# Performance work log

Measured on AMD Instinct MI355X. Metric: run time of the kernel, lower is better.

Reference implementation:

```python
import jax, jax.numpy as jnp
import numpy as np
import itertools

B, RES, RES_, STRIDE = 256, 14, 7, 2
N, N_ = RES * RES, RES_ * RES_
IN_DIM, OUT_DIM = 384, 512
H, KD, AR = 12, 32, 2
D = AR * KD            # 64, per-head value dim
DH = D * H             # 768
NH_KD = KD * H         # 384
KV_H = DH + NH_KD      # 1152
EPS = 1e-5


def _bias_idxs():
    # Replicates the relative-offset indexing from __init__.
    points = list(itertools.product(range(RES), range(RES)))
    points_ = list(itertools.product(range(RES_), range(RES_)))
    offsets, idxs = {}, []
    for p1 in points_:
        for p2 in points:
            off = (abs(p1[0] * STRIDE - p2[0]), abs(p1[1] * STRIDE - p2[1]))
            if off not in offsets:
                offsets[off] = len(offsets)
            idxs.append(offsets[off])
    return np.array(idxs, dtype=np.int32).reshape(N_, N), len(offsets)


def linear_bn(x, w, gamma, beta, mean, var):
    # Linear (no bias) followed by BatchNorm1d in inference form (fused affine).
    s = gamma / jnp.sqrt(var + EPS)
    return jnp.matmul(x, w.T) * s + (beta - mean * s)


def setup_inputs() -> dict:
    key = jax.random.key(0)
    ks = jax.random.split(key, 12)
    idxs_np, n_off = _bias_idxs()

    def bn_params(k, dim):
        k1, k2, k3, k4 = jax.random.split(k, 4)
        return (jax.random.normal(k1, (dim,)) * 0.1 + 1.0,   # gamma
                jax.random.normal(k2, (dim,)) * 0.1,          # beta
                jax.random.normal(k3, (dim,)) * 0.1,          # running_mean
                jax.random.uniform(k4, (dim,), minval=0.5, maxval=1.5))  # running_var

    kv_g, kv_b, kv_m, kv_v = bn_params(ks[1], KV_H)
    q_g, q_b, q_m, q_v = bn_params(ks[3], NH_KD)
    pr_g, pr_b, pr_m, pr_v = bn_params(ks[5], OUT_DIM)

    return {
        "x": jax.random.normal(ks[0], (B, N, IN_DIM), dtype=jnp.float32),
        "kv_w": jax.random.normal(ks[6], (KV_H, IN_DIM), dtype=jnp.float32) * (IN_DIM ** -0.5),
        "kv_g": kv_g, "kv_b": kv_b, "kv_m": kv_m, "kv_v": kv_v,
        "q_w": jax.random.normal(ks[7], (NH_KD, IN_DIM), dtype=jnp.float32) * (IN_DIM ** -0.5),
        "q_g": q_g, "q_b": q_b, "q_m": q_m, "q_v": q_v,
        "proj_w": jax.random.normal(ks[8], (OUT_DIM, DH), dtype=jnp.float32) * (DH ** -0.5),
        "proj_g": pr_g, "proj_b": pr_b, "proj_m": pr_m, "proj_v": pr_v,
        "attention_biases": jax.random.normal(ks[9], (H, n_off), dtype=jnp.float32) * 0.02,
        "bias_idxs": jnp.asarray(idxs_np),
    }


def reference(x, kv_w, kv_g, kv_b, kv_m, kv_v,
              q_w, q_g, q_b, q_m, q_v,
              proj_w, proj_g, proj_b, proj_m, proj_v,
              attention_biases, bias_idxs):
    Bsz = x.shape[0]
    scale = KD ** -0.5
    # kv projection: [B, N, H, KD+D] -> split into k, v
    kv = linear_bn(x, kv_w, kv_g, kv_b, kv_m, kv_v).reshape(Bsz, N, H, KD + D)
    k, v = kv[..., :KD], kv[..., KD:]
    # strided subsample of queries: [B, 14, 14, C] -> [B, 49, C]
    xs = x.reshape(Bsz, RES, RES, IN_DIM)[:, ::STRIDE, ::STRIDE].reshape(Bsz, N_, IN_DIM)
    q = linear_bn(xs, q_w, q_g, q_b, q_m, q_v).reshape(Bsz, N_, H, KD)
    # attention with gathered relative-position bias: bias [H, N_, N]
    bias = attention_biases[:, bias_idxs]
    attn = jnp.einsum('bqhd,bkhd->bhqk', q, k) * scale + bias
    attn = jax.nn.softmax(attn, axis=-1)
    out = jnp.einsum('bhqk,bkhd->bqhd', attn, v).reshape(Bsz, N_, DH)
    out = jax.nn.hard_swish(out)
    return linear_bn(out, proj_w, proj_g, proj_b, proj_m, proj_v)
```

## Files before the change

kernel.cpp:

```cpp
#include <hip/hip_runtime.h>
#include <hip/hip_bf16.h>
#include <math.h>

typedef unsigned short U16;
typedef unsigned int U32;
typedef __attribute__((ext_vector_type(8))) short bf8;
typedef __attribute__((ext_vector_type(4))) float f4;
typedef __attribute__((ext_vector_type(4))) unsigned short u16x4;

#define AS1 __attribute__((address_space(1)))
#define AS3 __attribute__((address_space(3)))

#define BSZ   256
#define NTOK  196
#define NQ    49
#define INDIM 384
#define OUTD  512
#define NH    12
#define DV    64
#define DHD   768
#define KVH   1152
#define NPADR 224

__device__ inline U16 f2bf(float f){
    __hip_bfloat16 h = __float2bfloat16(f);
    return *(U16*)&h;
}
__device__ inline f4 f4zero(){ f4 z; z[0]=0.f; z[1]=0.f; z[2]=0.f; z[3]=0.f; return z; }
__device__ inline bf8 bf8zero(){ bf8 v;
#pragma unroll
    for (int j=0;j<8;++j) v[j]=0; return v; }

__global__ void k_cast8p(const float* __restrict__ in, U16* __restrict__ out, int n8){
    int i = blockIdx.x*256 + threadIdx.x;
    if (i >= n8) return;
    int rall = i / 48;
    int c8   = i - rall*48;
    int b    = rall / NPADR;
    int r    = rall - b*NPADR;
    U16 o[8];
    if (r < NTOK){
        const float* p = in + ((size_t)(b*NTOK + r))*INDIM + c8*8;
#pragma unroll
        for (int j=0;j<8;++j) o[j] = f2bf(p[j]);
    } else {
#pragma unroll
        for (int j=0;j<8;++j) o[j] = 0;
    }
    *(bf8*)(out + (size_t)i*8) = *(const bf8*)o;
}

__global__ void k_castxs(const float* __restrict__ x, U16* __restrict__ out, int n8){
    int i = blockIdx.x*256 + threadIdx.x;
    if (i >= n8) return;
    int row = i / 48;
    int c8  = i - row*48;
    int b   = row / 49;
    int q   = row - b*49;
    int r_  = q / 7, c_ = q - r_*7;
    const float* p = x + ((size_t)(b*NTOK + 28*r_ + 2*c_))*INDIM + c8*8;
    U16 o[8];
#pragma unroll
    for (int j=0;j<8;++j) o[j] = f2bf(p[j]);
    *(bf8*)(out + (size_t)i*8) = *(const bf8*)o;
}

#define W1C (KVH*INDIM/8)
#define W2C (INDIM*INDIM/8)
#define W3C (OUTD*DHD/8)
__global__ void k_castw(const float* __restrict__ w1, const float* __restrict__ w2,
                        const float* __restrict__ w3, U16* __restrict__ o1,
                        U16* __restrict__ o2, U16* __restrict__ o3){
    int i = blockIdx.x*256 + threadIdx.x;
    const float* p; U16* o;
    if (i < W1C){ p = w1 + (size_t)i*8; o = o1 + (size_t)i*8; }
    else if (i < W1C+W2C){ int k=i-W1C; p = w2 + (size_t)k*8; o = o2 + (size_t)k*8; }
    else if (i < W1C+W2C+W3C){ int k=i-W1C-W2C; p = w3 + (size_t)k*8; o = o3 + (size_t)k*8; }
    else return;
    U16 t[8];
#pragma unroll
    for (int j=0;j<8;++j) t[j] = f2bf(p[j]);
    *(bf8*)o = *(const bf8*)t;
}

#define BIAS_N   (NH*NQ*NTOK)
#define BIAS_BLK ((BIAS_N+255)/256)
#define BN_BLK   ((KVH+INDIM+OUTD)/256)
__global__ void k_misc(const float* __restrict__ ab, const int* __restrict__ idxs, int n_off,
                       const float* __restrict__ g1, const float* __restrict__ b1,
                       const float* __restrict__ m1, const float* __restrict__ v1,
                       const float* __restrict__ g2, const float* __restrict__ b2,
                       const float* __restrict__ m2, const float* __restrict__ v2,
                       const float* __restrict__ g3, const float* __restrict__ b3,
                       const float* __restrict__ m3, const float* __restrict__ v3,
                       float* __restrict__ s1, float* __restrict__ bo1,
                       float* __restrict__ s2, float* __restrict__ bo2,
                       float* __restrict__ s3, float* __restrict__ bo3,
                       float* __restrict__ bias_out){
    int blk = blockIdx.x;
    int tid = threadIdx.x;
    if (blk < BIAS_BLK){
        int i = blk*256 + tid;
        if (i < BIAS_N){
            int h = i / (NQ*NTOK);
            int qk = i - h*(NQ*NTOK);
            bias_out[i] = ab[h*n_off + idxs[qk]];
        }
    } else {
        int i = (blk-BIAS_BLK)*256 + tid;
        const float *g,*b,*m,*v; float *so,*bo; int k;
        if (i < KVH){ g=g1;b=b1;m=m1;v=v1;so=s1;bo=bo1;k=i; }
        else if (i < KVH+INDIM){ g=g2;b=b2;m=m2;v=v2;so=s2;bo=bo2;k=i-KVH; }
        else { g=g3;b=b3;m=m3;v=v3;so=s3;bo=bo3;k=i-KVH-INDIM; }
        float s = g[k] / sqrtf(v[k] + 1e-5f);
        so[k] = s;
        bo[k] = b[k] - m[k]*s;
    }
}

#define KLO 12800
__global__ __launch_bounds__(256,2) void k_fused(
    const U16* __restrict__ xbf, const U16* __restrict__ kvw, const U16* __restrict__ qo_,
    const float* __restrict__ skv, const float* __restrict__ bkv,
    const float* __restrict__ biasf, U16* __restrict__ aout)
{
    __shared__ U16 smem[20480];
    const int hw = blockIdx.x;
    const int bh = (hw & 7)*384 + (hw >> 3);
    const int b = bh / NH, h = bh - b*NH;
    const int tid = threadIdx.x, lane = tid & 63, w = tid >> 6;
    const int wm = w & 1, wn = w >> 1;
    const int l15 = lane & 15, oct = lane >> 4;

    U16* Ab[2] = { smem + 0,     smem + 7168 };
    U16* Bb[2] = { smem + 14336, smem + 17408 };

    U32 aoff[4];
#pragma unroll
    for (int c=0;c<3;++c){
        int s = c*256 + tid;
        int ach = s / NPADR, ar = s - ach*NPADR;
        aoff[c] = (U32)(b*NPADR + ar)*INDIM + ach*8;
    }
    {
        int s = 768 + (tid & 127);
        int ach = s / NPADR, ar = s - ach*NPADR;
        aoff[3] = (U32)(b*NPADR + ar)*INDIM + ach*8;
    }
    U32 boff[2];
    {
        int s0 = tid;
        int bc0 = s0 / 96, br0 = s0 - bc0*96;
        boff[0] = (U32)(h*96 + br0)*INDIM + bc0*8;
        int s1 = 128 + (tid | 128);
        int bc1 = s1 / 96, br1 = s1 - bc1*96;
        boff[1] = (U32)(h*96 + br1)*INDIM + bc1*8;
    }

    f4 acc[7][3];
#pragma unroll
    for (int i=0;i<7;++i)
#pragma unroll
        for (int j=0;j<3;++j) acc[i][j] = f4zero();

#define STAGE(buf, kb) do{ \
    _Pragma("unroll") \
    for (int c=0;c<3;++c) \
        __builtin_amdgcn_global_load_lds((const AS1 U32*)(xbf + aoff[c] + (kb)), \
            (AS3 U32*)(Ab[buf] + (c*256+tid)*8), 16, 0, 0); \
    if (tid < 128) \
        __builtin_amdgcn_global_load_lds((const AS1 U32*)(xbf + aoff[3] + (kb)), \
            (AS3 U32*)(Ab[buf] + (768+tid)*8), 16, 0, 0); \
    __builtin_amdgcn_global_load_lds((const AS1 U32*)(kvw + boff[0] + (kb)), \
        (AS3 U32*)(Bb[buf] + tid*8), 16, 0, 0); \
    if (tid >= 128) \
        __builtin_amdgcn_global_load_lds((const AS1 U32*)(kvw + boff[1] + (kb)), \
            (AS3 U32*)(Bb[buf] + (128+tid)*8), 16, 0, 0); \
}while(0)

    STAGE(0, 0);

#pragma unroll
    for (int kt=0; kt<12; ++kt){
        const int cur = kt & 1;
        if (kt < 11){
            STAGE(cur^1, (kt+1)*32);
            asm volatile("s_waitcnt vmcnt(5)" ::: "memory");
        } else {
            asm volatile("s_waitcnt vmcnt(0)" ::: "memory");
        }
        __builtin_amdgcn_sched_barrier(0);
        __builtin_amdgcn_s_barrier();
        __builtin_amdgcn_sched_barrier(0);

        bf8 af[7], bfr[3];
#pragma unroll
        for (int i=0;i<7;++i)
            af[i]  = *(const bf8*)(Ab[cur] + (oct*NPADR + wm*112 + i*16 + l15)*8);
#pragma unroll
        for (int j=0;j<3;++j)
            bfr[j] = *(const bf8*)(Bb[cur] + (oct*96 + wn*48 + j*16 + l15)*8);
        __builtin_amdgcn_s_setprio(1);
#pragma unroll
        for (int i=0;i<7;++i)
#pragma unroll
            for (int j=0;j<3;++j)
                acc[i][j] = __builtin_amdgcn_mfma_f32_16x16x32_bf16(af[i], bfr[j], acc[i][j], 0, 0, 0);
        __builtin_amdgcn_s_setprio(0);
        __builtin_amdgcn_sched_barrier(0);
        __builtin_amdgcn_s_barrier();
        __builtin_amdgcn_sched_barrier(0);
    }
#undef STAGE

#pragma unroll
    for (int j=0;j<3;++j){
        const int cc = wn*48 + j*16 + l15;
        const float sc = skv[h*96 + cc];
        const float bi = bkv[h*96 + cc];
#pragma unroll
        for (int i=0;i<7;++i){
            const int n0 = wm*112 + i*16 + oct*4;
            if (cc < 32){
#pragma unroll
                for (int r=0;r<4;++r)
                    smem[KLO + ((cc>>3)*NPADR + n0 + r)*8 + (cc&7)] = f2bf(acc[i][j][r]*sc + bi);
            } else if (n0 < 200){
                const int dv = cc - 32;
                u16x4 pk;
#pragma unroll
                for (int r=0;r<4;++r) pk[r] = f2bf(acc[i][j][r]*sc + bi);
                *(u16x4*)(smem + ((n0>>3)*64 + dv)*8 + (oct&1)*4) = pk;
            }
        }
    }
    __syncthreads();

    const int qg = w*16 + l15;
    bf8 qf = bf8zero();
    if (qg < NQ) qf = *(const bf8*)(qo_ + ((size_t)(b*NQ + qg))*INDIM + h*32 + oct*8);

    f4 sacc[14];
#pragma unroll
    for (int mt=0;mt<14;++mt) sacc[mt] = f4zero();
#pragma unroll
    for (int mt=0;mt<14;++mt){
        const bf8 kf = *(const bf8*)(smem + KLO + (oct*NPADR + mt*16 + l15)*8);
        sacc[mt] = __builtin_amdgcn_mfma_f32_16x16x32_bf16(kf, qf, sacc[mt], 0, 0, 0);
    }

    const float scale = 0.17677669529663689f;
    float mx = -1e30f;
#pragma unroll
    for (int mt=0;mt<14;++mt){
        const int n0 = mt*16 + oct*4;
        f4 bi4 = f4zero();
        if (qg < NQ && n0 < NTOK) bi4 = *(const f4*)(biasf + ((size_t)h*NQ + qg)*NTOK + n0);
#pragma unroll
        for (int r=0;r<4;++r){
            float s = (n0 + r < NTOK) ? sacc[mt][r]*scale + bi4[r] : -1e30f;
            sacc[mt][r] = s;
            mx = fmaxf(mx, s);
        }
    }
    mx = fmaxf(mx, __shfl_xor(mx, 16));
    mx = fmaxf(mx, __shfl_xor(mx, 32));

    float sum = 0.f;
#pragma unroll
    for (int mt=0;mt<14;++mt){
#pragma unroll
        for (int r=0;r<4;++r){
            float p = (mt*16 + oct*4 + r < NTOK) ? __expf(sacc[mt][r] - mx) : 0.f;
            sacc[mt][r] = p;
            sum += p;
        }
    }
    sum += __shfl_xor(sum, 16);
    sum += __shfl_xor(sum, 32);
    const float inv = 1.f / sum;

    const int src1 = l15 + (oct & 1)*32;
    const int src2 = src1 + 16;
    const bool hiT = (oct >> 1) != 0;
    f4 pacc[4];
#pragma unroll
    for (int dt=0;dt<4;++dt) pacc[dt] = f4zero();
#pragma unroll
    for (int kt=0;kt<7;++kt){
        const int m0 = 2*kt, m1 = 2*kt+1;
        U32 q00 = (U32)f2bf(sacc[m0][0]*inv) | ((U32)f2bf(sacc[m0][1]*inv) << 16);
        U32 q01 = (U32)f2bf(sacc[m0][2]*inv) | ((U32)f2bf(sacc[m0][3]*inv) << 16);
        U32 q10 = (U32)f2bf(sacc[m1][0]*inv) | ((U32)f2bf(sacc[m1][1]*inv) << 16);
        U32 q11 = (U32)f2bf(sacc[m1][2]*inv) | ((U32)f2bf(sacc[m1][3]*inv) << 16);
        U32 a0 = __shfl(q00, src1), a1 = __shfl(q01, src1);
        U32 c0 = __shfl(q10, src1), c1 = __shfl(q11, src1);
        U32 b0 = __shfl(q00, src2), b1 = __shfl(q01, src2);
        U32 d0 = __shfl(q10, src2), d1 = __shfl(q11, src2);
        union { U32 u[4]; bf8 v; } pu;
        pu.u[0] = hiT ? c0 : a0;
        pu.u[1] = hiT ? c1 : a1;
        pu.u[2] = hiT ? d0 : b0;
        pu.u[3] = hiT ? d1 : b1;
#pragma unroll
        for (int dt=0;dt<4;++dt){
            const bf8 vf = *(const bf8*)(smem + ((kt*4 + oct)*64 + dt*16 + l15)*8);
            pacc[dt] = __builtin_amdgcn_mfma_f32_16x16x32_bf16(pu.v, vf, pacc[dt], 0, 0, 0);
        }
    }

#pragma unroll
    for (int dt=0;dt<4;++dt){
#pragma unroll
        for (int r=0;r<4;++r){
            const int qo2 = w*16 + oct*4 + r;
            if (qo2 < NQ){
                const int d = dt*16 + l15;
                float v = pacc[dt][r];
                float tt = fminf(fmaxf(v + 3.f, 0.f), 6.f);
                aout[((size_t)(b*NQ + qo2))*DHD + h*DV + d] = f2bf(v * tt * (1.f/6.f));
            }
        }
    }
}

__global__ __launch_bounds__(256,2) void k_qgemm(
    const U16* __restrict__ A, const U16* __restrict__ Bw,
    const float* __restrict__ s_arr, const float* __restrict__ b_arr,
    U16* __restrict__ o16)
{
    __shared__ U16 smem[32768];
    U16* Ab[2] = { smem,          smem + 8192 };
    U16* Bb[2] = { smem + 16384,  smem + 24576 };
    const int gn0 = blockIdx.x * 128;
    const int gm0 = blockIdx.y * 128;
    const int tid  = threadIdx.x;
    const int lane = tid & 63;
    const int w    = tid >> 6;
    const int wm   = w >> 1, wn = w & 1;
    const int l15  = lane & 15, oct = lane >> 4;

    f4 acc[4][4];
#pragma unroll
    for (int i=0;i<4;++i)
#pragma unroll
        for (int j=0;j<4;++j) acc[i][j] = f4zero();

    size_t aoff[4], boff[4];
#pragma unroll
    for (int c=0;c<4;++c){
        int slot = c*256 + tid;
        int row = slot & 127, ch = slot >> 7;
        aoff[c] = (size_t)(gm0 + row)*INDIM + ch*8;
        boff[c] = (size_t)(gn0 + row)*INDIM + ch*8;
    }

#pragma unroll
    for (int c=0;c<4;++c){
        __builtin_amdgcn_global_load_lds((const AS1 U32*)(A + aoff[c]),
            (AS3 U32*)(Ab[0] + (c*256+tid)*8), 16, 0, 0);
        __builtin_amdgcn_global_load_lds((const AS1 U32*)(Bw + boff[c]),
            (AS3 U32*)(Bb[0] + (c*256+tid)*8), 16, 0, 0);
    }

#pragma unroll
    for (int kt=0; kt<6; ++kt){
        const int cur = kt & 1;
        if (kt+1 < 6){
            const int kb = (kt+1)*64;
#pragma unroll
            for (int c=0;c<4;++c){
                __builtin_amdgcn_global_load_lds((const AS1 U32*)(A + aoff[c] + kb),
                    (AS3 U32*)(Ab[cur^1] + (c*256+tid)*8), 16, 0, 0);
                __builtin_amdgcn_global_load_lds((const AS1 U32*)(Bw + boff[c] + kb),
                    (AS3 U32*)(Bb[cur^1] + (c*256+tid)*8), 16, 0, 0);
            }
            asm volatile("s_waitcnt vmcnt(8)" ::: "memory");
        } else {
            asm volatile("s_waitcnt vmcnt(0)" ::: "memory");
        }
        __builtin_amdgcn_sched_barrier(0);
        __builtin_amdgcn_s_barrier();
        __builtin_amdgcn_sched_barrier(0);

#pragma unroll
        for (int kk=0;kk<2;++kk){
            bf8 af[4], bfr[4];
#pragma unroll
            for (int i=0;i<4;++i)
                af[i]  = *(const bf8*)(Ab[cur] + ((kk*4+oct)*128 + wm*64 + i*16 + l15)*8);
#pragma unroll
            for (int j=0;j<4;++j)
                bfr[j] = *(const bf8*)(Bb[cur] + ((kk*4+oct)*128 + wn*64 + j*16 + l15)*8);
            __builtin_amdgcn_s_setprio(1);
#pragma unroll
            for (int i=0;i<4;++i)
#pragma unroll
                for (int j=0;j<4;++j)
                    acc[i][j] = __builtin_amdgcn_mfma_f32_16x16x32_bf16(af[i], bfr[j], acc[i][j], 0, 0, 0);
            __builtin_amdgcn_s_setprio(0);
        }
        __builtin_amdgcn_sched_barrier(0);
        __builtin_amdgcn_s_barrier();
        __builtin_amdgcn_sched_barrier(0);
    }

#pragma unroll
    for (int j=0;j<4;++j){
        const int col = gn0 + wn*64 + j*16 + l15;
        const float sc = s_arr[col];
        const float bi = b_arr[col];
#pragma unroll
        for (int i=0;i<4;++i){
            const int row0 = gm0 + wm*64 + i*16 + oct*4;
#pragma unroll
            for (int r=0;r<4;++r)
                o16[(size_t)(row0+r)*INDIM + col] = f2bf(acc[i][j][r]*sc + bi);
        }
    }
}

__global__ __launch_bounds__(256,2) void k_proj(
    const U16* __restrict__ A, const U16* __restrict__ Bw,
    const float* __restrict__ s_arr, const float* __restrict__ b_arr,
    float* __restrict__ o32)
{
    __shared__ U16 smem[32768];
    U16* Ab[2] = { smem,          smem + 8192 };
    U16* Bb[2] = { smem + 16384,  smem + 24576 };
    const int l   = (blockIdx.x & 7)*49 + (blockIdx.x >> 3);
    const int gn0 = (l & 3) * 128;
    const int gm0 = (l >> 2) * 128;
    const int tid  = threadIdx.x;
    const int lane = tid & 63;
    const int w    = tid >> 6;
    const int wm   = w >> 1, wn = w & 1;
    const int l15  = lane & 15, oct = lane >> 4;

    f4 acc[4][4];
#pragma unroll
    for (int i=0;i<4;++i)
#pragma unroll
        for (int j=0;j<4;++j) acc[i][j] = f4zero();

    size_t aoff[4], boff[4];
#pragma unroll
    for (int c=0;c<4;++c){
        int slot = c*256 + tid;
        int row = slot & 127, ch = slot >> 7;
        aoff[c] = (size_t)(gm0 + row)*DHD + ch*8;
        boff[c] = (size_t)(gn0 + row)*DHD + ch*8;
    }

#pragma unroll
    for (int c=0;c<4;++c){
        __builtin_amdgcn_global_load_lds((const AS1 U32*)(A + aoff[c]),
            (AS3 U32*)(Ab[0] + (c*256+tid)*8), 16, 0, 0);
        __builtin_amdgcn_global_load_lds((const AS1 U32*)(Bw + boff[c]),
            (AS3 U32*)(Bb[0] + (c*256+tid)*8), 16, 0, 0);
    }

#pragma unroll
    for (int kt=0; kt<12; ++kt){
        const int cur = kt & 1;
        if (kt+1 < 12){
            const int kb = (kt+1)*64;
#pragma unroll
            for (int c=0;c<4;++c){
                __builtin_amdgcn_global_load_lds((const AS1 U32*)(A + aoff[c] + kb),
                    (AS3 U32*)(Ab[cur^1] + (c*256+tid)*8), 16, 0, 0);
                __builtin_amdgcn_global_load_lds((const AS1 U32*)(Bw + boff[c] + kb),
                    (AS3 U32*)(Bb[cur^1] + (c*256+tid)*8), 16, 0, 0);
            }
            asm volatile("s_waitcnt vmcnt(8)" ::: "memory");
        } else {
            asm volatile("s_waitcnt vmcnt(0)" ::: "memory");
        }
        __builtin_amdgcn_sched_barrier(0);
        __builtin_amdgcn_s_barrier();
        __builtin_amdgcn_sched_barrier(0);

#pragma unroll
        for (int kk=0;kk<2;++kk){
            bf8 af[4], bfr[4];
#pragma unroll
            for (int i=0;i<4;++i)
                af[i]  = *(const bf8*)(Ab[cur] + ((kk*4+oct)*128 + wm*64 + i*16 + l15)*8);
#pragma unroll
            for (int j=0;j<4;++j)
                bfr[j] = *(const bf8*)(Bb[cur] + ((kk*4+oct)*128 + wn*64 + j*16 + l15)*8);
            __builtin_amdgcn_s_setprio(1);
#pragma unroll
            for (int i=0;i<4;++i)
#pragma unroll
                for (int j=0;j<4;++j)
                    acc[i][j] = __builtin_amdgcn_mfma_f32_16x16x32_bf16(af[i], bfr[j], acc[i][j], 0, 0, 0);
            __builtin_amdgcn_s_setprio(0);
        }
        __builtin_amdgcn_sched_barrier(0);
        __builtin_amdgcn_s_barrier();
        __builtin_amdgcn_sched_barrier(0);
    }

#pragma unroll
    for (int j=0;j<4;++j){
        const int col = gn0 + wn*64 + j*16 + l15;
        const float sc = s_arr[col];
        const float bi = b_arr[col];
#pragma unroll
        for (int i=0;i<4;++i){
            const int row0 = gm0 + wm*64 + i*16 + oct*4;
#pragma unroll
            for (int r=0;r<4;++r)
                o32[(size_t)(row0+r)*OUTD + col] = acc[i][j][r]*sc + bi;
        }
    }
}

extern "C" void kernel_launch(void* const* d_in, const int* in_sizes, int n_in,
                              void* d_out, int out_size, void* d_ws, size_t ws_size,
                              hipStream_t stream)
{
    const float* x    = (const float*)d_in[0];
    const float* kv_w = (const float*)d_in[1];
    const float* kv_g = (const float*)d_in[2];
    const float* kv_b = (const float*)d_in[3];
    const float* kv_m = (const float*)d_in[4];
    const float* kv_v = (const float*)d_in[5];
    const float* q_w  = (const float*)d_in[6];
    const float* q_g  = (const float*)d_in[7];
    const float* q_b  = (const float*)d_in[8];
    const float* q_m  = (const float*)d_in[9];
    const float* q_v  = (const float*)d_in[10];
    const float* pr_w = (const float*)d_in[11];
    const float* pr_g = (const float*)d_in[12];
    const float* pr_b = (const float*)d_in[13];
    const float* pr_m = (const float*)d_in[14];
    const float* pr_v = (const float*)d_in[15];
    const float* ab   = (const float*)d_in[16];
    const int*  idxs  = (const int*)d_in[17];
    const int n_off = in_sizes[16] / NH;

    char* ws = (char*)d_ws;
    size_t off = 0;
    auto alloc = [&](size_t bytes)->char*{
        char* p = ws + off; off += (bytes + 255) & ~(size_t)255; return p;
    };
    U16*   x_bf   = (U16*)  alloc((size_t)BSZ*NPADR*INDIM*2);
    U16*   xs_bf  = (U16*)  alloc((size_t)BSZ*NQ*INDIM*2);
    U16*   kvw_bf = (U16*)  alloc((size_t)KVH*INDIM*2);
    U16*   qw_bf  = (U16*)  alloc((size_t)INDIM*INDIM*2);
    U16*   prw_bf = (U16*)  alloc((size_t)OUTD*DHD*2);
    float* s_kv   = (float*)alloc(KVH*4);
    float* b_kv   = (float*)alloc(KVH*4);
    float* s_q    = (float*)alloc(INDIM*4);
    float* b_q    = (float*)alloc(INDIM*4);
    float* s_pr   = (float*)alloc(OUTD*4);
    float* b_pr   = (float*)alloc(OUTD*4);
    float* biasf  = (float*)alloc(((size_t)NH*NQ*NTOK + 256)*4);
    U16*   q_out  = (U16*)  alloc((size_t)BSZ*NQ*INDIM*2);
    U16*   a_out  = (U16*)  alloc((size_t)BSZ*NQ*DHD*2);
    if (off > ws_size) return;

    {
        int n8 = BSZ*NPADR*INDIM/8;
        k_cast8p<<<(n8+255)/256, 256, 0, stream>>>(x, x_bf, n8);
    }
    {
        int n8 = BSZ*NQ*INDIM/8;
        k_castxs<<<(n8+255)/256, 256, 0, stream>>>(x, xs_bf, n8);
    }
    k_castw<<<(W1C+W2C+W3C+255)/256, 256, 0, stream>>>(kv_w, q_w, pr_w, kvw_bf, qw_bf, prw_bf);
    k_misc<<<BIAS_BLK+BN_BLK, 256, 0, stream>>>(
        ab, idxs, n_off,
        kv_g, kv_b, kv_m, kv_v, q_g, q_b, q_m, q_v, pr_g, pr_b, pr_m, pr_v,
        s_kv, b_kv, s_q, b_q, s_pr, b_pr, biasf);

    {
        dim3 g(INDIM/128, BSZ*NQ/128);
        k_qgemm<<<g, 256, 0, stream>>>(xs_bf, qw_bf, s_q, b_q, q_out);
    }
    k_fused<<<BSZ*NH, 256, 0, stream>>>(x_bf, kvw_bf, q_out, s_kv, b_kv, biasf, a_out);
    k_proj<<<392, 256, 0, stream>>>(a_out, prw_bf, s_pr, b_pr, (float*)d_out);
}
```

Before: 191.3 us.

## Unify q and proj GEMMs into 128x64-tile template, fold query subsampling into loads

```diff
diff --git a/kernel.cpp b/kernel.cpp
--- a/kernel.cpp
+++ b/kernel.cpp
@@ -47,21 +47,6 @@
 #pragma unroll
         for (int j=0;j<8;++j) o[j] = 0;
     }
-    *(bf8*)(out + (size_t)i*8) = *(const bf8*)o;
-}
-
-__global__ void k_castxs(const float* __restrict__ x, U16* __restrict__ out, int n8){
-    int i = blockIdx.x*256 + threadIdx.x;
-    if (i >= n8) return;
-    int row = i / 48;
-    int c8  = i - row*48;
-    int b   = row / 49;
-    int q   = row - b*49;
-    int r_  = q / 7, c_ = q - r_*7;
-    const float* p = x + ((size_t)(b*NTOK + 28*r_ + 2*c_))*INDIM + c8*8;
-    U16 o[8];
-#pragma unroll
-    for (int j=0;j<8;++j) o[j] = f2bf(p[j]);
     *(bf8*)(out + (size_t)i*8) = *(const bf8*)o;
 }
 
@@ -324,58 +309,70 @@
     }
 }
 
-__global__ __launch_bounds__(256,2) void k_qgemm(
+template<int EPI, int NK, int KD, int NTILN, int NWG, bool SUB>
+__global__ __launch_bounds__(256,2) void k_g64(
     const U16* __restrict__ A, const U16* __restrict__ Bw,
     const float* __restrict__ s_arr, const float* __restrict__ b_arr,
-    U16* __restrict__ o16)
+    U16* __restrict__ o16, float* __restrict__ o32)
 {
-    __shared__ U16 smem[32768];
+    __shared__ U16 smem[24576];
     U16* Ab[2] = { smem,          smem + 8192 };
-    U16* Bb[2] = { smem + 16384,  smem + 24576 };
-    const int gn0 = blockIdx.x * 128;
-    const int gm0 = blockIdx.y * 128;
+    U16* Bb[2] = { smem + 16384,  smem + 20480 };
+    constexpr int QQ = NWG/8, RR = NWG%8;
+    const int xcd = blockIdx.x & 7, rest = blockIdx.x >> 3;
+    const int l = (xcd < RR ? xcd*(QQ+1) : RR*(QQ+1) + (xcd-RR)*QQ) + rest;
+    const int mtl = l / NTILN, ntl = l - mtl*NTILN;
+    const int gm0 = mtl*128, gn0 = ntl*64;
     const int tid  = threadIdx.x;
     const int lane = tid & 63;
     const int w    = tid >> 6;
-    const int wm   = w >> 1, wn = w & 1;
+    const int wm   = w & 1, wn = w >> 1;
     const int l15  = lane & 15, oct = lane >> 4;
 
-    f4 acc[4][4];
+    f4 acc[4][2];
 #pragma unroll
     for (int i=0;i<4;++i)
 #pragma unroll
-        for (int j=0;j<4;++j) acc[i][j] = f4zero();
-
-    size_t aoff[4], boff[4];
+        for (int j=0;j<2;++j) acc[i][j] = f4zero();
+
+    U32 aoff[4], boff[2];
 #pragma unroll
     for (int c=0;c<4;++c){
         int slot = c*256 + tid;
         int row = slot & 127, ch = slot >> 7;
-        aoff[c] = (size_t)(gm0 + row)*INDIM + ch*8;
-        boff[c] = (size_t)(gn0 + row)*INDIM + ch*8;
-    }
-
-#pragma unroll
-    for (int c=0;c<4;++c){
-        __builtin_amdgcn_global_load_lds((const AS1 U32*)(A + aoff[c]),
-            (AS3 U32*)(Ab[0] + (c*256+tid)*8), 16, 0, 0);
-        __builtin_amdgcn_global_load_lds((const AS1 U32*)(Bw + boff[c]),
-            (AS3 U32*)(Bb[0] + (c*256+tid)*8), 16, 0, 0);
-    }
-
-#pragma unroll
-    for (int kt=0; kt<6; ++kt){
+        int grow = gm0 + row;
+        if (SUB){
+            int b2 = grow / NQ, qq = grow - b2*NQ;
+            grow = b2*NPADR + 28*(qq/7) + 2*(qq%7);
+        }
+        aoff[c] = (U32)grow*KD + ch*8;
+    }
+#pragma unroll
+    for (int c=0;c<2;++c){
+        int slot = c*256 + tid;
+        int row = slot & 63, ch = slot >> 6;
+        boff[c] = (U32)(gn0 + row)*KD + ch*8;
+    }
+
+#define STG(buf, kb) do{ \
+    _Pragma("unroll") \
+    for (int c=0;c<4;++c) \
+        __builtin_amdgcn_global_load_lds((const AS1 U32*)(A + aoff[c] + (kb)), \
+            (AS3 U32*)(Ab[buf] + (c*256+tid)*8), 16, 0, 0); \
+    _Pragma("unroll") \
+    for (int c=0;c<2;++c) \
+        __builtin_amdgcn_global_load_lds((const AS1 U32*)(Bw + boff[c] + (kb)), \
+            (AS3 U32*)(Bb[buf] + (c*256+tid)*8), 16, 0, 0); \
+}while(0)
+
+    STG(0, 0);
+
+#pragma unroll
+    for (int kt=0; kt<NK; ++kt){
         const int cur = kt & 1;
-        if (kt+1 < 6){
-            const int kb = (kt+1)*64;
-#pragma unroll
-            for (int c=0;c<4;++c){
-                __builtin_amdgcn_global_load_lds((const AS1 U32*)(A + aoff[c] + kb),
-                    (AS3 U32*)(Ab[cur^1] + (c*256+tid)*8), 16, 0, 0);
-                __builtin_amdgcn_global_load_lds((const AS1 U32*)(Bw + boff[c] + kb),
-                    (AS3 U32*)(Bb[cur^1] + (c*256+tid)*8), 16, 0, 0);
-            }
-            asm volatile("s_waitcnt vmcnt(8)" ::: "memory");
+        if (kt+1 < NK){
+            STG(cur^1, (kt+1)*64);
+            asm volatile("s_waitcnt vmcnt(6)" ::: "memory");
         } else {
             asm volatile("s_waitcnt vmcnt(0)" ::: "memory");
         }
@@ -385,18 +382,18 @@
 
 #pragma unroll
         for (int kk=0;kk<2;++kk){
-            bf8 af[4], bfr[4];
+            bf8 af[4], bfr[2];
 #pragma unroll
             for (int i=0;i<4;++i)
                 af[i]  = *(const bf8*)(Ab[cur] + ((kk*4+oct)*128 + wm*64 + i*16 + l15)*8);
 #pragma unroll
-            for (int j=0;j<4;++j)
-                bfr[j] = *(const bf8*)(Bb[cur] + ((kk*4+oct)*128 + wn*64 + j*16 + l15)*8);
+            for (int j=0;j<2;++j)
+                bfr[j] = *(const bf8*)(Bb[cur] + ((kk*4+oct)*64 + wn*32 + j*16 + l15)*8);
             __builtin_amdgcn_s_setprio(1);
 #pragma unroll
             for (int i=0;i<4;++i)
 #pragma unroll
-                for (int j=0;j<4;++j)
+                for (int j=0;j<2;++j)
                     acc[i][j] = __builtin_amdgcn_mfma_f32_16x16x32_bf16(af[i], bfr[j], acc[i][j], 0, 0, 0);
             __builtin_amdgcn_s_setprio(0);
         }
@@ -404,115 +401,22 @@
         __builtin_amdgcn_s_barrier();
         __builtin_amdgcn_sched_barrier(0);
     }
-
-#pragma unroll
-    for (int j=0;j<4;++j){
-        const int col = gn0 + wn*64 + j*16 + l15;
+#undef STG
+
+#pragma unroll
+    for (int j=0;j<2;++j){
+        const int col = gn0 + wn*32 + j*16 + l15;
         const float sc = s_arr[col];
         const float bi = b_arr[col];
 #pragma unroll
         for (int i=0;i<4;++i){
             const int row0 = gm0 + wm*64 + i*16 + oct*4;
 #pragma unroll
-            for (int r=0;r<4;++r)
-                o16[(size_t)(row0+r)*INDIM + col] = f2bf(acc[i][j][r]*sc + bi);
-        }
-    }
-}
-
-__global__ __launch_bounds__(256,2) void k_proj(
-    const U16* __restrict__ A, const U16* __restrict__ Bw,
-    const float* __restrict__ s_arr, const float* __restrict__ b_arr,
-    float* __restrict__ o32)
-{
-    __shared__ U16 smem[32768];
-    U16* Ab[2] = { smem,          smem + 8192 };
-    U16* Bb[2] = { smem + 16384,  smem + 24576 };
-    const int l   = (blockIdx.x & 7)*49 + (blockIdx.x >> 3);
-    const int gn0 = (l & 3) * 128;
-    const int gm0 = (l >> 2) * 128;
-    const int tid  = threadIdx.x;
-    const int lane = tid & 63;
-    const int w    = tid >> 6;
-    const int wm   = w >> 1, wn = w & 1;
-    const int l15  = lane & 15, oct = lane >> 4;
-
-    f4 acc[4][4];
-#pragma unroll
-    for (int i=0;i<4;++i)
-#pragma unroll
-        for (int j=0;j<4;++j) acc[i][j] = f4zero();
-
-    size_t aoff[4], boff[4];
-#pragma unroll
-    for (int c=0;c<4;++c){
-        int slot = c*256 + tid;
-        int row = slot & 127, ch = slot >> 7;
-        aoff[c] = (size_t)(gm0 + row)*DHD + ch*8;
-        boff[c] = (size_t)(gn0 + row)*DHD + ch*8;
-    }
-
-#pragma unroll
-    for (int c=0;c<4;++c){
-        __builtin_amdgcn_global_load_lds((const AS1 U32*)(A + aoff[c]),
-            (AS3 U32*)(Ab[0] + (c*256+tid)*8), 16, 0, 0);
-        __builtin_amdgcn_global_load_lds((const AS1 U32*)(Bw + boff[c]),
-            (AS3 U32*)(Bb[0] + (c*256+tid)*8), 16, 0, 0);
-    }
-
-#pragma unroll
-    for (int kt=0; kt<12; ++kt){
-        const int cur = kt & 1;
-        if (kt+1 < 12){
-            const int kb = (kt+1)*64;
-#pragma unroll
-            for (int c=0;c<4;++c){
-                __builtin_amdgcn_global_load_lds((const AS1 U32*)(A + aoff[c] + kb),
-                    (AS3 U32*)(Ab[cur^1] + (c*256+tid)*8), 16, 0, 0);
-                __builtin_amdgcn_global_load_lds((const AS1 U32*)(Bw + boff[c] + kb),
-                    (AS3 U32*)(Bb[cur^1] + (c*256+tid)*8), 16, 0, 0);
+            for (int r=0;r<4;++r){
+                const float val = acc[i][j][r]*sc + bi;
+                if (EPI == 0) o16[(size_t)(row0+r)*INDIM + col] = f2bf(val);
+                else          o32[(size_t)(row0+r)*OUTD  + col] = val;
             }
-            asm volatile("s_waitcnt vmcnt(8)" ::: "memory");
-        } else {
-            asm volatile("s_waitcnt vmcnt(0)" ::: "memory");
-        }
-        __builtin_amdgcn_sched_barrier(0);
-        __builtin_amdgcn_s_barrier();
-        __builtin_amdgcn_sched_barrier(0);
-
-#pragma unroll
-        for (int kk=0;kk<2;++kk){
-            bf8 af[4], bfr[4];
-#pragma unroll
-            for (int i=0;i<4;++i)
-                af[i]  = *(const bf8*)(Ab[cur] + ((kk*4+oct)*128 + wm*64 + i*16 + l15)*8);
-#pragma unroll
-            for (int j=0;j<4;++j)
-                bfr[j] = *(const bf8*)(Bb[cur] + ((kk*4+oct)*128 + wn*64 + j*16 + l15)*8);
-            __builtin_amdgcn_s_setprio(1);
-#pragma unroll
-            for (int i=0;i<4;++i)
-#pragma unroll
-                for (int j=0;j<4;++j)
-                    acc[i][j] = __builtin_amdgcn_mfma_f32_16x16x32_bf16(af[i], bfr[j], acc[i][j], 0, 0, 0);
-            __builtin_amdgcn_s_setprio(0);
-        }
-        __builtin_amdgcn_sched_barrier(0);
-        __builtin_amdgcn_s_barrier();
-        __builtin_amdgcn_sched_barrier(0);
-    }
-
-#pragma unroll
-    for (int j=0;j<4;++j){
-        const int col = gn0 + wn*64 + j*16 + l15;
-        const float sc = s_arr[col];
-        const float bi = b_arr[col];
-#pragma unroll
-        for (int i=0;i<4;++i){
-            const int row0 = gm0 + wm*64 + i*16 + oct*4;
-#pragma unroll
-            for (int r=0;r<4;++r)
-                o32[(size_t)(row0+r)*OUTD + col] = acc[i][j][r]*sc + bi;
         }
     }
 }
@@ -547,7 +451,6 @@
         char* p = ws + off; off += (bytes + 255) & ~(size_t)255; return p;
     };
     U16*   x_bf   = (U16*)  alloc((size_t)BSZ*NPADR*INDIM*2);
-    U16*   xs_bf  = (U16*)  alloc((size_t)BSZ*NQ*INDIM*2);
     U16*   kvw_bf = (U16*)  alloc((size_t)KVH*INDIM*2);
     U16*   qw_bf  = (U16*)  alloc((size_t)INDIM*INDIM*2);
     U16*   prw_bf = (U16*)  alloc((size_t)OUTD*DHD*2);
@@ -566,20 +469,15 @@
         int n8 = BSZ*NPADR*INDIM/8;
         k_cast8p<<<(n8+255)/256, 256, 0, stream>>>(x, x_bf, n8);
     }
-    {
-        int n8 = BSZ*NQ*INDIM/8;
-        k_castxs<<<(n8+255)/256, 256, 0, stream>>>(x, xs_bf, n8);
-    }
     k_castw<<<(W1C+W2C+W3C+255)/256, 256, 0, stream>>>(kv_w, q_w, pr_w, kvw_bf, qw_bf, prw_bf);
     k_misc<<<BIAS_BLK+BN_BLK, 256, 0, stream>>>(
         ab, idxs, n_off,
         kv_g, kv_b, kv_m, kv_v, q_g, q_b, q_m, q_v, pr_g, pr_b, pr_m, pr_v,
         s_kv, b_kv, s_q, b_q, s_pr, b_pr, biasf);
 
-    {
-        dim3 g(INDIM/128, BSZ*NQ/128);
-        k_qgemm<<<g, 256, 0, stream>>>(xs_bf, qw_bf, s_q, b_q, q_out);
-    }
+    k_g64<0, 6, INDIM, 6, 588, true><<<588, 256, 0, stream>>>(
+        x_bf, qw_bf, s_q, b_q, q_out, nullptr);
     k_fused<<<BSZ*NH, 256, 0, stream>>>(x_bf, kvw_bf, q_out, s_kv, b_kv, biasf, a_out);
-    k_proj<<<392, 256, 0, stream>>>(a_out, prw_bf, s_pr, b_pr, (float*)d_out);
-}
+    k_g64<1, 12, DHD, 8, 784, false><<<784, 256, 0, stream>>>(
+        a_out, prw_bf, s_pr, b_pr, nullptr, (float*)d_out);
+}
```

Measured after the change: 192.0 us. About the same (+0.4%).
